# Optimization experiments

Measured on AMD Instinct MI355X. Metric: run time of the kernel, lower is better.

## Reference

```python
import jax, jax.numpy as jnp
import numpy as np

EMBED = 1024

def setup_inputs() -> dict:
    key = jax.random.key(0)
    kx, kq, kk, kv = jax.random.split(key, 4)
    x = jax.random.normal(kx, (4, 2048, EMBED), dtype=jnp.float32)
    s = 1.0 / np.sqrt(EMBED)
    Wq = jax.random.normal(kq, (EMBED, EMBED), dtype=jnp.float32) * s
    Wk = jax.random.normal(kk, (EMBED, EMBED), dtype=jnp.float32) * s
    Wv = jax.random.normal(kv, (EMBED, EMBED), dtype=jnp.float32) * s
    return {"x": x, "Wq": Wq, "Wk": Wk, "Wv": Wv}

def reference(x, Wq, Wk, Wv):
    # x: [b, s, e]; nn.Linear(y) = y @ W.T, weights stored [out, in]
    Q = jnp.einsum('bse,oe->bso', x, Wq)
    K = jnp.einsum('bse,oe->bso', x, Wk)
    V = jnp.einsum('bse,oe->bso', x, Wv)
    scale = 1.0 / jnp.sqrt(jnp.asarray(x.shape[-1], x.dtype))
    energy = jnp.einsum('bqe,bke->bqk', Q, K) * scale  # [b, s, s]
    attention = jax.nn.softmax(energy, axis=-1)
    out = jnp.einsum('bqk,bke->bqe', attention, V)
    return out
```

## Files before the change

kernel.cpp:

```cpp
#include <hip/hip_runtime.h>
#include <stdint.h>


typedef __attribute__((ext_vector_type(8))) short bf16x8;
typedef __attribute__((ext_vector_type(4))) float f32x4;

__device__ __forceinline__ float bf2f(uint16_t u) {
    return __uint_as_float(((uint32_t)u) << 16);
}
__device__ __forceinline__ uint16_t f2bf(float f) {
    uint32_t u = __float_as_uint(f);
    uint32_t r = u + 0x7FFFu + ((u >> 16) & 1u);
    return (uint16_t)(r >> 16);
}

__device__ __forceinline__ void gll16(const void* g, void* l) {
    __builtin_amdgcn_global_load_lds(
        (const __attribute__((address_space(1))) uint32_t*)g,
        (__attribute__((address_space(3))) uint32_t*)l,
        16, 0, 0);
}

__global__ __launch_bounds__(256) void cast_f32_bf16(const float* __restrict__ in,
                                                     uint16_t* __restrict__ out,
                                                     int n4) {
    int i = blockIdx.x * 256 + threadIdx.x;
    if (i < n4) {
        float4 v = ((const float4*)in)[i];
        ushort4 o;
        o.x = f2bf(v.x); o.y = f2bf(v.y); o.z = f2bf(v.z); o.w = f2bf(v.w);
        ((ushort4*)out)[i] = o;
    }
}

__global__ __launch_bounds__(256) void transpose_bf16(const uint16_t* __restrict__ in,
                                                      uint16_t* __restrict__ out,
                                                      int rows, int cols, int istride,
                                                      long ibatch, long obatch) {
    __shared__ uint16_t tile[32][33];
    in  += (long)blockIdx.z * ibatch;
    out += (long)blockIdx.z * obatch;
    int bx = blockIdx.x * 32;
    int by = blockIdx.y * 32;
    int tx = threadIdx.x, ty = threadIdx.y;
    #pragma unroll
    for (int i = ty; i < 32; i += 8)
        tile[i][tx] = in[(long)(by + i) * istride + bx + tx];
    __syncthreads();
    #pragma unroll
    for (int i = ty; i < 32; i += 8)
        out[(long)(bx + i) * rows + by + tx] = tile[tx][i];
}

__global__ __launch_bounds__(256) void softmax_rows(uint16_t* __restrict__ P) {
    const int n = 2048;
    uint16_t* row = P + (size_t)blockIdx.x * n;
    int tid = threadIdx.x;
    int w = tid >> 6, ln = tid & 63;
    float v[8];
    float m = -3.4e38f;
    #pragma unroll
    for (int i = 0; i < 8; i++) { v[i] = bf2f(row[tid + 256 * i]); m = fmaxf(m, v[i]); }
    #pragma unroll
    for (int o = 32; o >= 1; o >>= 1) m = fmaxf(m, __shfl_down(m, o, 64));
    __shared__ float smax[4], ssum[4];
    if (ln == 0) smax[w] = m;
    __syncthreads();
    m = fmaxf(fmaxf(smax[0], smax[1]), fmaxf(smax[2], smax[3]));
    float s = 0.f;
    #pragma unroll
    for (int i = 0; i < 8; i++) { v[i] = __expf(v[i] - m); s += v[i]; }
    #pragma unroll
    for (int o = 32; o >= 1; o >>= 1) s += __shfl_down(s, o, 64);
    if (ln == 0) ssum[w] = s;
    __syncthreads();
    s = ssum[0] + ssum[1] + ssum[2] + ssum[3];
    float inv = 1.f / s;
    #pragma unroll
    for (int i = 0; i < 8; i++) row[tid + 256 * i] = f2bf(v[i] * inv);
}

#define BM 128
#define BN 128
#define BK 32

template <typename OutT>
__global__ __launch_bounds__(256) void gemm_nt(const uint16_t* __restrict__ A,
                                               const uint16_t* __restrict__ B,
                                               OutT* __restrict__ C,
                                               int gx, int gy,
                                               long lda, long ldb, long ldc,
                                               int K, float alpha,
                                               long sA, long sB, long sC) {
    const int total = gridDim.x;
    const int n     = blockIdx.x;
    const int per   = total >> 3;
    const int g     = (n & 7) * per + (n >> 3);
    const int pb    = gx * gy;
    const int bz    = g / pb;
    const int r     = g - bz * pb;
    const int stpr  = gx >> 3;
    const int st    = r >> 6;
    const int w     = r & 63;
    const int sty   = st / stpr;
    const int stx   = st - sty * stpr;
    const int bx    = (stx << 3) + (w & 7);
    const int by    = (sty << 3) + (w >> 3);

    A += (long)bz * sA;
    B += (long)bz * sB;
    C += (long)bz * sC;

    __shared__ uint16_t As[3][BM * BK];
    __shared__ uint16_t Bs[3][BM * BK];

    const int tid  = threadIdx.x;
    const int m0   = by * BM;
    const int n0   = bx * BN;
    const int wave = tid >> 6;
    const int lane = tid & 63;
    const int quad = lane >> 4;
    const int l16  = lane & 15;
    const int wr   = (wave >> 1) * 64;
    const int wc   = (wave & 1) * 64;

    const int sr = tid >> 2;
    const int sc = (tid & 3) * 8;
    const uint16_t* Ag = A + (long)(m0 + sr) * lda + sc;
    const uint16_t* Bg = B + (long)(n0 + sr) * ldb + sc;
    const long rsA = 64 * lda;
    const long rsB = 64 * ldb;
    const int so0 = sr * BK + sc;
    const int so1 = (sr + 64) * BK + sc;

    const int nk = K / BK;

    gll16(Ag,       &As[0][so0]);
    gll16(Ag + rsA, &As[0][so1]);
    gll16(Bg,       &Bs[0][so0]);
    gll16(Bg + rsB, &Bs[0][so1]);
    Ag += BK; Bg += BK;
    gll16(Ag,       &As[1][so0]);
    gll16(Ag + rsA, &As[1][so1]);
    gll16(Bg,       &Bs[1][so0]);
    gll16(Bg + rsB, &Bs[1][so1]);
    Ag += BK; Bg += BK;

    f32x4 acc[4][4] = {};
    int cur = 0, pf = 2;

    for (int k = 0; k < nk; ++k) {
        if (k < nk - 1) {
            asm volatile("s_waitcnt vmcnt(4)\n\ts_barrier" ::: "memory");
        } else {
            asm volatile("s_waitcnt vmcnt(0)\n\ts_barrier" ::: "memory");
        }

        if (k + 2 < nk) {
            gll16(Ag,       &As[pf][so0]);
            gll16(Ag + rsA, &As[pf][so1]);
            gll16(Bg,       &Bs[pf][so0]);
            gll16(Bg + rsB, &Bs[pf][so1]);
            Ag += BK; Bg += BK;
        }

        const uint16_t* Ac = As[cur];
        const uint16_t* Bc = Bs[cur];
        const int ko = quad * 8;
        bf16x8 af[4], bfr[4];
        #pragma unroll
        for (int i = 0; i < 4; i++)
            af[i] = *(const bf16x8*)(&Ac[(wr + i * 16 + l16) * BK + ko]);
        #pragma unroll
        for (int j = 0; j < 4; j++)
            bfr[j] = *(const bf16x8*)(&Bc[(wc + j * 16 + l16) * BK + ko]);
        #pragma unroll
        for (int i = 0; i < 4; i++)
            #pragma unroll
            for (int j = 0; j < 4; j++)
                acc[i][j] = __builtin_amdgcn_mfma_f32_16x16x32_bf16(af[i], bfr[j], acc[i][j], 0, 0, 0);

        cur = (cur == 2) ? 0 : cur + 1;
        pf  = (pf  == 2) ? 0 : pf + 1;
    }

    #pragma unroll
    for (int i = 0; i < 4; i++) {
        #pragma unroll
        for (int j = 0; j < 4; j++) {
            #pragma unroll
            for (int r4 = 0; r4 < 4; r4++) {
                int row = m0 + wr + i * 16 + quad * 4 + r4;
                int col = n0 + wc + j * 16 + l16;
                float val = acc[i][j][r4] * alpha;
                if constexpr (sizeof(OutT) == 2)
                    C[(long)row * ldc + col] = f2bf(val);
                else
                    C[(long)row * ldc + col] = val;
            }
        }
    }
}

extern "C" void kernel_launch(void* const* d_in, const int* in_sizes, int n_in,
                              void* d_out, int out_size, void* d_ws, size_t ws_size,
                              hipStream_t stream) {
    const float* x  = (const float*)d_in[0];
    const float* Wq = (const float*)d_in[1];
    const float* Wk = (const float*)d_in[2];
    const float* Wv = (const float*)d_in[3];
    float* out = (float*)d_out;

    const int Bn = 4, S = 2048, E = 1024;
    const long MS = (long)Bn * S;
    const int  N3 = 3 * E;

    char* ws = (char*)d_ws;
    uint16_t* xb    = (uint16_t*)ws;  ws += (size_t)MS * E * 2;
    uint16_t* wqkvb = (uint16_t*)ws;  ws += (size_t)N3 * E * 2;
    uint16_t* QKVb  = (uint16_t*)ws;  ws += (size_t)MS * N3 * 2;
    uint16_t* Pb    = (uint16_t*)ws;  ws += (size_t)Bn * S * S * 2;
    uint16_t* Vt    = (uint16_t*)ws;  ws += (size_t)Bn * E * S * 2;

    dim3 blk(256);

    {
        int n4 = (int)(MS * E / 4);
        cast_f32_bf16<<<dim3((n4 + 255) / 256), blk, 0, stream>>>(x, xb, n4);
        int n4w = E * E / 4;
        dim3 gw((n4w + 255) / 256);
        cast_f32_bf16<<<gw, blk, 0, stream>>>(Wq, wqkvb,             n4w);
        cast_f32_bf16<<<gw, blk, 0, stream>>>(Wk, wqkvb + (size_t)E * E,     n4w);
        cast_f32_bf16<<<gw, blk, 0, stream>>>(Wv, wqkvb + (size_t)2 * E * E, n4w);
    }

    {
        int gx = N3 / BN, gy = (int)(MS / BM);
        gemm_nt<uint16_t><<<dim3(gx * gy), blk, 0, stream>>>(
            xb, wqkvb, QKVb, gx, gy, E, E, N3, E, 1.f, 0, 0, 0);
    }

    transpose_bf16<<<dim3(E / 32, S / 32, Bn), dim3(32, 8), 0, stream>>>(
        QKVb + 2 * E, Vt, S, E, N3, (long)S * N3, (long)E * S);

    {
        int gx = S / BN, gy = S / BM;
        gemm_nt<uint16_t><<<dim3(gx * gy * Bn), blk, 0, stream>>>(
            QKVb, QKVb + E, Pb, gx, gy, N3, N3, S, E, 0.03125f,
            (long)S * N3, (long)S * N3, (long)S * S);
    }

    softmax_rows<<<dim3(Bn * S), blk, 0, stream>>>(Pb);

    {
        int gx = E / BN, gy = S / BM;
        gemm_nt<float><<<dim3(gx * gy * Bn), blk, 0, stream>>>(
            Pb, Vt, out, gx, gy, S, S, E, S, 1.f,
            (long)S * S, (long)E * S, (long)S * E);
    }
}
```

Before: 278.6 us.

## Load GEMM A operand directly from global into registers, keep only B in LDS

The A tile is no longer staged through shared memory with global_load_lds. Each wave now reads its A fragments straight from global memory into registers every k-step, and only B stays triple-buffered in LDS. The B load mapping is rearranged per wave and the wait count is lowered to match. This frees half the LDS and drops the A LDS round-trip, but the A loads are no longer prefetched, so their global latency sits right before the MFMAs. A rows are also now fetched separately by the two waves that share them.

```diff
diff --git a/kernel.cpp b/kernel.cpp
--- a/kernel.cpp
+++ b/kernel.cpp
@@ -111,8 +111,7 @@
     B += (long)bz * sB;
     C += (long)bz * sC;
 
-    __shared__ uint16_t As[3][BM * BK];
-    __shared__ uint16_t Bs[3][BM * BK];
+    __shared__ uint16_t Bs[3][BN * BK];
 
     const int tid  = threadIdx.x;
     const int m0   = by * BM;
@@ -124,53 +123,48 @@
     const int wr   = (wave >> 1) * 64;
     const int wc   = (wave & 1) * 64;
 
-    const int sr = tid >> 2;
-    const int sc = (tid & 3) * 8;
-    const uint16_t* Ag = A + (long)(m0 + sr) * lda + sc;
-    const uint16_t* Bg = B + (long)(n0 + sr) * ldb + sc;
-    const long rsA = 64 * lda;
-    const long rsB = 64 * ldb;
-    const int so0 = sr * BK + sc;
-    const int so1 = (sr + 64) * BK + sc;
+    const int gB0 = 2 * wave;
+    const uint16_t* Bg0 = B + (long)(n0 + gB0 * 16 + (lane >> 2)) * ldb + (lane & 3) * 8;
+    const uint16_t* Bg1 = Bg0 + 16 * ldb;
+    const int bo0 = gB0 * 512;
+    const int bo1 = bo0 + 512;
+
+    const uint16_t* Ap[4];
+    #pragma unroll
+    for (int i = 0; i < 4; i++)
+        Ap[i] = A + (long)(m0 + wr + i * 16 + l16) * lda + quad * 8;
 
     const int nk = K / BK;
 
-    gll16(Ag,       &As[0][so0]);
-    gll16(Ag + rsA, &As[0][so1]);
-    gll16(Bg,       &Bs[0][so0]);
-    gll16(Bg + rsB, &Bs[0][so1]);
-    Ag += BK; Bg += BK;
-    gll16(Ag,       &As[1][so0]);
-    gll16(Ag + rsA, &As[1][so1]);
-    gll16(Bg,       &Bs[1][so0]);
-    gll16(Bg + rsB, &Bs[1][so1]);
-    Ag += BK; Bg += BK;
+    gll16(Bg0, &Bs[0][bo0]);
+    gll16(Bg1, &Bs[0][bo1]);
+    gll16(Bg0 + BK, &Bs[1][bo0]);
+    gll16(Bg1 + BK, &Bs[1][bo1]);
 
     f32x4 acc[4][4] = {};
     int cur = 0, pf = 2;
+    long kb = 2 * BK;
 
     for (int k = 0; k < nk; ++k) {
-        if (k < nk - 1) {
-            asm volatile("s_waitcnt vmcnt(4)\n\ts_barrier" ::: "memory");
-        } else {
-            asm volatile("s_waitcnt vmcnt(0)\n\ts_barrier" ::: "memory");
+        asm volatile("s_waitcnt vmcnt(2)\n\ts_barrier" ::: "memory");
+
+        bf16x8 af[4];
+        #pragma unroll
+        for (int i = 0; i < 4; i++)
+            af[i] = *(const bf16x8*)(Ap[i]);
+        #pragma unroll
+        for (int i = 0; i < 4; i++)
+            Ap[i] += BK;
+
+        if (k + 2 < nk) {
+            gll16(Bg0 + kb, &Bs[pf][bo0]);
+            gll16(Bg1 + kb, &Bs[pf][bo1]);
+            kb += BK;
         }
 
-        if (k + 2 < nk) {
-            gll16(Ag,       &As[pf][so0]);
-            gll16(Ag + rsA, &As[pf][so1]);
-            gll16(Bg,       &Bs[pf][so0]);
-            gll16(Bg + rsB, &Bs[pf][so1]);
-            Ag += BK; Bg += BK;
-        }
-
-        const uint16_t* Ac = As[cur];
         const uint16_t* Bc = Bs[cur];
         const int ko = quad * 8;
-        bf16x8 af[4], bfr[4];
-        #pragma unroll
-        for (int i = 0; i < 4; i++)
-            af[i] = *(const bf16x8*)(&Ac[(wr + i * 16 + l16) * BK + ko]);
+        bf16x8 bfr[4];
         #pragma unroll
         for (int j = 0; j < 4; j++)
             bfr[j] = *(const bf16x8*)(&Bc[(wc + j * 16 + l16) * BK + ko]);
```

After: 402.6 us. 1.45x slower.

## Fuse V transpose into QKV GEMM epilogue and merge cast kernels

Applied to the files above, without the earlier changes.

The QKV projection GEMM now writes the V third of its output directly in transposed [b, e, s] layout, using 4-element vector stores along the sequence dimension. This removes the separate transpose kernel and its extra round trip of V through global memory. Q and K are stored in a narrower 2048-column buffer. The four f32-to-bf16 cast launches are merged into one kernel to cut launch overhead. The transposed stores are strided by 2048 elements across lanes, so that epilogue may coalesce poorly.

```diff
diff --git a/kernel.cpp b/kernel.cpp
--- a/kernel.cpp
+++ b/kernel.cpp
@@ -21,35 +21,31 @@
         16, 0, 0);
 }
 
-__global__ __launch_bounds__(256) void cast_f32_bf16(const float* __restrict__ in,
-                                                     uint16_t* __restrict__ out,
-                                                     int n4) {
+__global__ __launch_bounds__(256) void cast_all(const float* __restrict__ x,
+                                                const float* __restrict__ Wq,
+                                                const float* __restrict__ Wk,
+                                                const float* __restrict__ Wv,
+                                                uint16_t* __restrict__ xb,
+                                                uint16_t* __restrict__ wqkvb,
+                                                int NX4, int NW4) {
     int i = blockIdx.x * 256 + threadIdx.x;
-    if (i < n4) {
-        float4 v = ((const float4*)in)[i];
-        ushort4 o;
-        o.x = f2bf(v.x); o.y = f2bf(v.y); o.z = f2bf(v.z); o.w = f2bf(v.w);
-        ((ushort4*)out)[i] = o;
-    }
-}
-
-__global__ __launch_bounds__(256) void transpose_bf16(const uint16_t* __restrict__ in,
-                                                      uint16_t* __restrict__ out,
-                                                      int rows, int cols, int istride,
-                                                      long ibatch, long obatch) {
-    __shared__ uint16_t tile[32][33];
-    in  += (long)blockIdx.z * ibatch;
-    out += (long)blockIdx.z * obatch;
-    int bx = blockIdx.x * 32;
-    int by = blockIdx.y * 32;
-    int tx = threadIdx.x, ty = threadIdx.y;
-    #pragma unroll
-    for (int i = ty; i < 32; i += 8)
-        tile[i][tx] = in[(long)(by + i) * istride + bx + tx];
-    __syncthreads();
-    #pragma unroll
-    for (int i = ty; i < 32; i += 8)
-        out[(long)(bx + i) * rows + by + tx] = tile[tx][i];
+    const float* src;
+    uint16_t* dst;
+    int off;
+    if (i < NX4) {
+        src = x; dst = xb; off = i;
+    } else {
+        int j = i - NX4;
+        if (j >= 3 * NW4) return;
+        int which = j / NW4;
+        off = j - which * NW4;
+        src = (which == 0) ? Wq : (which == 1) ? Wk : Wv;
+        dst = wqkvb + (size_t)which * NW4 * 4;
+    }
+    float4 v = ((const float4*)src)[off];
+    ushort4 o;
+    o.x = f2bf(v.x); o.y = f2bf(v.y); o.z = f2bf(v.z); o.w = f2bf(v.w);
+    ((ushort4*)dst)[off] = o;
 }
 
 __global__ __launch_bounds__(256) void softmax_rows(uint16_t* __restrict__ P) {
@@ -91,7 +87,9 @@
                                                int gx, int gy,
                                                long lda, long ldb, long ldc,
                                                int K, float alpha,
-                                               long sA, long sB, long sC) {
+                                               long sA, long sB, long sC,
+                                               uint16_t* __restrict__ VtP,
+                                               int vcol0) {
     const int total = gridDim.x;
     const int n     = blockIdx.x;
     const int per   = total >> 3;
@@ -184,19 +182,38 @@
         pf  = (pf  == 2) ? 0 : pf + 1;
     }
 
-    #pragma unroll
-    for (int i = 0; i < 4; i++) {
-        #pragma unroll
-        for (int j = 0; j < 4; j++) {
+    if (VtP && n0 >= vcol0) {
+        #pragma unroll
+        for (int i = 0; i < 4; i++) {
+            const int row0 = m0 + wr + i * 16 + quad * 4;
+            const int b    = row0 >> 11;
+            const int s    = row0 & 2047;
             #pragma unroll
-            for (int r4 = 0; r4 < 4; r4++) {
-                int row = m0 + wr + i * 16 + quad * 4 + r4;
-                int col = n0 + wc + j * 16 + l16;
-                float val = acc[i][j][r4] * alpha;
-                if constexpr (sizeof(OutT) == 2)
-                    C[(long)row * ldc + col] = f2bf(val);
-                else
-                    C[(long)row * ldc + col] = val;
+            for (int j = 0; j < 4; j++) {
+                const int e = n0 + wc + j * 16 + l16 - vcol0;
+                ushort4 o;
+                o.x = f2bf(acc[i][j][0]);
+                o.y = f2bf(acc[i][j][1]);
+                o.z = f2bf(acc[i][j][2]);
+                o.w = f2bf(acc[i][j][3]);
+                *(ushort4*)(VtP + ((long)b * 1024 + e) * 2048 + s) = o;
+            }
+        }
+    } else {
+        #pragma unroll
+        for (int i = 0; i < 4; i++) {
+            #pragma unroll
+            for (int j = 0; j < 4; j++) {
+                #pragma unroll
+                for (int r4 = 0; r4 < 4; r4++) {
+                    int row = m0 + wr + i * 16 + quad * 4 + r4;
+                    int col = n0 + wc + j * 16 + l16;
+                    float val = acc[i][j][r4] * alpha;
+                    if constexpr (sizeof(OutT) == 2)
+                        C[(long)row * ldc + col] = f2bf(val);
+                    else
+                        C[(long)row * ldc + col] = val;
+                }
             }
         }
     }
@@ -218,36 +235,33 @@
     char* ws = (char*)d_ws;
     uint16_t* xb    = (uint16_t*)ws;  ws += (size_t)MS * E * 2;
     uint16_t* wqkvb = (uint16_t*)ws;  ws += (size_t)N3 * E * 2;
-    uint16_t* QKVb  = (uint16_t*)ws;  ws += (size_t)MS * N3 * 2;
+    uint16_t* QKb   = (uint16_t*)ws;  ws += (size_t)MS * 2048 * 2;
+    uint16_t* Vt    = (uint16_t*)ws;  ws += (size_t)Bn * E * S * 2;
     uint16_t* Pb    = (uint16_t*)ws;  ws += (size_t)Bn * S * S * 2;
-    uint16_t* Vt    = (uint16_t*)ws;  ws += (size_t)Bn * E * S * 2;
 
     dim3 blk(256);
 
     {
-        int n4 = (int)(MS * E / 4);
-        cast_f32_bf16<<<dim3((n4 + 255) / 256), blk, 0, stream>>>(x, xb, n4);
-        int n4w = E * E / 4;
-        dim3 gw((n4w + 255) / 256);
-        cast_f32_bf16<<<gw, blk, 0, stream>>>(Wq, wqkvb,             n4w);
-        cast_f32_bf16<<<gw, blk, 0, stream>>>(Wk, wqkvb + (size_t)E * E,     n4w);
-        cast_f32_bf16<<<gw, blk, 0, stream>>>(Wv, wqkvb + (size_t)2 * E * E, n4w);
+        int NX4 = (int)(MS * E / 4);
+        int NW4 = E * E / 4;
+        int tot = NX4 + 3 * NW4;
+        cast_all<<<dim3((tot + 255) / 256), blk, 0, stream>>>(
+            x, Wq, Wk, Wv, xb, wqkvb, NX4, NW4);
     }
 
     {
         int gx = N3 / BN, gy = (int)(MS / BM);
         gemm_nt<uint16_t><<<dim3(gx * gy), blk, 0, stream>>>(
-            xb, wqkvb, QKVb, gx, gy, E, E, N3, E, 1.f, 0, 0, 0);
-    }
-
-    transpose_bf16<<<dim3(E / 32, S / 32, Bn), dim3(32, 8), 0, stream>>>(
-        QKVb + 2 * E, Vt, S, E, N3, (long)S * N3, (long)E * S);
+            xb, wqkvb, QKb, gx, gy, E, E, 2048, E, 1.f, 0, 0, 0,
+            Vt, 2048);
+    }
 
     {
         int gx = S / BN, gy = S / BM;
         gemm_nt<uint16_t><<<dim3(gx * gy * Bn), blk, 0, stream>>>(
-            QKVb, QKVb + E, Pb, gx, gy, N3, N3, S, E, 0.03125f,
-            (long)S * N3, (long)S * N3, (long)S * S);
+            QKb, QKb + 1024, Pb, gx, gy, 2048, 2048, S, E, 0.03125f,
+            (long)S * 2048, (long)S * 2048, (long)S * S,
+            nullptr, 0);
     }
 
     softmax_rows<<<dim3(Bn * S), blk, 0, stream>>>(Pb);
@@ -256,6 +270,7 @@
         int gx = E / BN, gy = S / BM;
         gemm_nt<float><<<dim3(gx * gy * Bn), blk, 0, stream>>>(
             Pb, Vt, out, gx, gy, S, S, E, S, 1.f,
-            (long)S * S, (long)E * S, (long)S * E);
-    }
-}
+            (long)S * S, (long)E * S, (long)S * E,
+            nullptr, 0);
+    }
+}
```

New measurement: 264.6 us. 1.05x faster.
